# Optimization experiments

Hardware: AMD Instinct MI355X
Metric: run time of the kernel (lower is better)

The kernel has to match this reference:

```python
import jax, jax.numpy as jnp
import numpy as np

B, N, F_IN, F_OUT, OUT = 32, 1024, 128, 128, 1


def setup_inputs() -> dict:
    key = jax.random.key(0)
    k = jax.random.split(key, 6)
    A = jax.random.uniform(k[0], (B, N, N), dtype=jnp.float32)
    H = jax.random.normal(k[1], (B, N, F_IN), dtype=jnp.float32)
    W = jax.random.normal(k[2], (F_IN, F_OUT), dtype=jnp.float32)
    b = jax.random.normal(k[3], (F_OUT,), dtype=jnp.float32)
    fc_w = jax.random.normal(k[4], (OUT, F_OUT), dtype=jnp.float32)
    fc_b = jax.random.normal(k[5], (OUT,), dtype=jnp.float32)
    return {"A": A, "H": H, "W": W, "b": b, "fc_w": fc_w, "fc_b": fc_b}


def reference(A, H, W, b, fc_w, fc_b):
    n = A.shape[1]
    A_tilde = A + jnp.eye(n, dtype=A.dtype)          # [B,N,N] add self-loops
    d = jnp.sum(A_tilde, axis=1)                      # [B,N] degrees (col sums, matches torch dim=1)
    inv_sqrt_d = 1.0 / jnp.sqrt(d)                    # elementwise, equivalent to sqrt(inv(diag(d)))
    # D^-1/2 A_tilde D^-1/2 as row/col scaling (avoids diag_embed + matrix inverse)
    A_norm = inv_sqrt_d[:, :, None] * A_tilde * inv_sqrt_d[:, None, :]
    h = jax.nn.relu(jnp.einsum('bij,bjf,fo->bio', A_norm, H, W) + b)  # GCN layer
    pooled = jnp.sum(h, axis=1)                       # [B,F_OUT] sum pooling over nodes
    return pooled @ fc_w.T + fc_b                     # [B,OUT]
```

## Files before the change

kernel.cpp:

```cpp
#include <hip/hip_runtime.h>
#include <hip/hip_bf16.h>

#define NB 32
#define NN 1024
#define FF 128

typedef __attribute__((ext_vector_type(8))) short short8;
typedef __attribute__((ext_vector_type(4))) float f32x4;

static __device__ __forceinline__ unsigned short f2bf(float x) {
  unsigned int u = __float_as_uint(x);
  u += 0x7fffu + ((u >> 16) & 1u);
  return (unsigned short)(u >> 16);
}

static __device__ __forceinline__ unsigned long long pack4bf(float a, float b, float c, float d) {
  return (unsigned long long)f2bf(a)
       | ((unsigned long long)f2bf(b) << 16)
       | ((unsigned long long)f2bf(c) << 32)
       | ((unsigned long long)f2bf(d) << 48);
}

static __device__ __forceinline__ void gl16(const void* g, void* l) {
  __builtin_amdgcn_global_load_lds((const __attribute__((address_space(1))) void*)g,
                                   (__attribute__((address_space(3))) void*)l, 16, 0, 0);
}

__global__ __launch_bounds__(256) void k1_colsum_cvt(const float* __restrict__ A,
                                                     unsigned short* __restrict__ Ab,
                                                     float* __restrict__ partial) {
  int t = threadIdx.x;
  int s = blockIdx.x;
  int b = blockIdx.y;
  const float* base = A + (size_t)b * NN * NN + (size_t)(s * 64) * NN + (t << 2);
  unsigned short* obase = Ab + (size_t)b * NN * NN + (size_t)(s * 64) * NN + (t << 2);
  int jj = t << 2;
  bool diag_band = ((t >> 4) == s);
  float4 sum = make_float4(0.f, 0.f, 0.f, 0.f);
  #pragma unroll 8
  for (int i = 0; i < 64; ++i) {
    float4 v = *reinterpret_cast<const float4*>(base + (size_t)i * NN);
    if (diag_band) {
      int gi = (s << 6) + i;
      v.x += (gi == jj)     ? 1.f : 0.f;
      v.y += (gi == jj + 1) ? 1.f : 0.f;
      v.z += (gi == jj + 2) ? 1.f : 0.f;
      v.w += (gi == jj + 3) ? 1.f : 0.f;
    }
    sum.x += v.x; sum.y += v.y; sum.z += v.z; sum.w += v.w;
    *reinterpret_cast<unsigned long long*>(obase + (size_t)i * NN) =
        pack4bf(v.x, v.y, v.z, v.w);
  }
  *reinterpret_cast<float4*>(partial + (((b << 4) + s) << 10) + jj) = sum;
}

__global__ __launch_bounds__(512) void k3_hw(const float* __restrict__ H,
                                             const float* __restrict__ W,
                                             const float* __restrict__ partial,
                                             unsigned short* __restrict__ HWpT) {
  __shared__ unsigned short Ws[128][136];
  __shared__ unsigned short Hs[128][136];
  __shared__ float isdJ[128];
  int jblk = blockIdx.x;
  int b = blockIdx.y;
  int tid = threadIdx.x, wave = tid >> 6, lane = tid & 63;

  if (tid < 128) {
    float d = 0.f;
    #pragma unroll
    for (int s = 0; s < 16; ++s) d += partial[(((b << 4) + s) << 10) + (jblk << 7) + tid];
    isdJ[tid] = rsqrtf(d);
  }
  #pragma unroll
  for (int p = 0; p < 8; ++p) {
    int idx = (p << 11) + (tid << 2);
    int k = idx >> 7, o = idx & 127;
    const float4 w = *reinterpret_cast<const float4*>(W + idx);
    Ws[o    ][k] = f2bf(w.x);
    Ws[o + 1][k] = f2bf(w.y);
    Ws[o + 2][k] = f2bf(w.z);
    Ws[o + 3][k] = f2bf(w.w);
  }
  {
    int r = tid >> 5, c = (tid & 31) << 2;
    const float* Hbase = H + (size_t)b * NN * FF + (size_t)(jblk * 128) * FF;
    #pragma unroll
    for (int p = 0; p < 8; ++p) {
      int row = r + (p << 4);
      const float4 v = *reinterpret_cast<const float4*>(Hbase + (size_t)row * FF + c);
      *reinterpret_cast<unsigned long long*>(&Hs[row][c]) = pack4bf(v.x, v.y, v.z, v.w);
    }
  }
  __syncthreads();

  f32x4 acc[8];
  #pragma unroll
  for (int i = 0; i < 8; ++i) acc[i] = (f32x4){0.f, 0.f, 0.f, 0.f};

  int mrow = (wave << 4) + (lane & 15);
  int koff = (lane >> 4) << 3;
  #pragma unroll
  for (int kk = 0; kk < 4; ++kk) {
    short8 af = *reinterpret_cast<const short8*>(&Ws[mrow][(kk << 5) + koff]);
    #pragma unroll
    for (int nf = 0; nf < 8; ++nf) {
      short8 bf = *reinterpret_cast<const short8*>(&Hs[(nf << 4) + (lane & 15)][(kk << 5) + koff]);
      acc[nf] = __builtin_amdgcn_mfma_f32_16x16x32_bf16(af, bf, acc[nf], 0, 0, 0);
    }
  }

  int q = lane >> 4, l15 = lane & 15;
  __syncthreads();
  #pragma unroll
  for (int nf = 0; nf < 8; ++nf) {
    int jl = (nf << 4) + l15;
    float sc = isdJ[jl];
    #pragma unroll
    for (int r = 0; r < 4; ++r) {
      Ws[(wave << 4) + (q << 2) + r][jl] = f2bf(acc[nf][r] * sc);
    }
  }
  __syncthreads();
  {
    unsigned short* obase = HWpT + (size_t)b * FF * NN + (size_t)(jblk * 128);
    int c8 = (tid & 15) << 3;
    #pragma unroll
    for (int p = 0; p < 4; ++p) {
      int o = (p << 5) + (tid >> 4);
      *reinterpret_cast<short8*>(obase + (size_t)o * NN + c8) =
          *reinterpret_cast<const short8*>(&Ws[o][c8]);
    }
  }
}

__global__ __launch_bounds__(256) void k4_gcn(const unsigned short* __restrict__ Ab,
                                              const unsigned short* __restrict__ HWpT,
                                              const float* __restrict__ partial,
                                              const float* __restrict__ bias,
                                              float* __restrict__ pooled_part) {
  __shared__ __align__(1024) char ldsA[3 * 8192];
  __shared__ __align__(16) float ldsIsd[64];
  __shared__ float ldsRed[2][128];
  int fid = blockIdx.x;
  int nid = (fid & 7) * 64 + (fid >> 3);
  int b = nid >> 4, iblk = nid & 15;
  int i0 = iblk << 6;
  int tid = threadIdx.x, wave = tid >> 6, lane = tid & 63;
  int wm = wave >> 1, wn = wave & 1;
  int l15 = lane & 15, q = lane >> 4;
  int q16 = q << 4;

  if (tid < 64) {
    float d = 0.f;
    #pragma unroll
    for (int s = 0; s < 16; ++s) d += partial[(((b << 4) + s) << 10) + i0 + tid];
    ldsIsd[tid] = rsqrtf(d);
  }

  int r8 = lane >> 3;
  int ch = (lane & 7) ^ r8;
  const unsigned short* aS = Ab + (size_t)b * NN * NN
                           + (size_t)(i0 + (wave << 4) + r8) * NN + (ch << 3);
  const unsigned short* bS = HWpT + (size_t)b * FF * NN
                           + (size_t)((wn << 6) + l15) * NN + (q << 3);

  f32x4 acc[2][4];
  #pragma unroll
  for (int m = 0; m < 2; ++m)
    #pragma unroll
    for (int n = 0; n < 4; ++n) acc[m][n] = (f32x4){0.f, 0.f, 0.f, 0.f};

  int swzR = (l15 & 7) << 4;
  int offA[2];
  #pragma unroll
  for (int mr = 0; mr < 2; ++mr)
    offA[mr] = ((wm << 5) + (mr << 4) + l15) * 128 + q16;

  short8 breg[2][4][2];

#define STAGE_A(buf, k0) { \
    const unsigned short* s_ = aS + (k0); \
    char* d_ = ldsA + (buf) * 8192 + (wave << 11); \
    gl16(s_,          d_); \
    gl16(s_ + 8 * NN, d_ + 1024); }

#define LOAD_B(slot, k0) { \
    _Pragma("unroll") \
    for (int nf_ = 0; nf_ < 4; ++nf_) { \
      _Pragma("unroll") \
      for (int kk_ = 0; kk_ < 2; ++kk_) \
        breg[slot][nf_][kk_] = *reinterpret_cast<const short8*>( \
            bS + (size_t)(nf_ << 4) * NN + (k0) + (kk_ << 5)); } }

  STAGE_A(0, 0)
  LOAD_B(0, 0)
  STAGE_A(1, 64)

  #pragma unroll
  for (int t = 0; t < 16; ++t) {
    if (t < 15) LOAD_B((t + 1) & 1, (t + 1) * 64)
    if (t < 14) STAGE_A((t + 2) % 3, (t + 2) * 64)
    if (t < 14)       asm volatile("s_waitcnt vmcnt(12)" ::: "memory");
    else if (t == 14) asm volatile("s_waitcnt vmcnt(10)" ::: "memory");
    else              asm volatile("s_waitcnt vmcnt(0)" ::: "memory");
    __builtin_amdgcn_s_barrier();
    const char* Abuf = ldsA + (t % 3) * 8192;
    #pragma unroll
    for (int kk = 0; kk < 2; ++kk) {
      short8 af[2];
      #pragma unroll
      for (int mr = 0; mr < 2; ++mr)
        af[mr] = *reinterpret_cast<const short8*>(Abuf + ((offA[mr] + (kk << 6)) ^ swzR));
      #pragma unroll
      for (int mr = 0; mr < 2; ++mr)
        #pragma unroll
        for (int nf = 0; nf < 4; ++nf)
          acc[mr][nf] = __builtin_amdgcn_mfma_f32_16x16x32_bf16(
              af[mr], breg[t & 1][nf][kk], acc[mr][nf], 0, 0, 0);
    }
    __builtin_amdgcn_s_barrier();
  }
#undef STAGE_A
#undef LOAD_B

  #pragma unroll
  for (int nf = 0; nf < 4; ++nf) {
    int f = (wn << 6) + (nf << 4) + l15;
    float bi = bias[f];
    float stot = 0.f;
    #pragma unroll
    for (int mr = 0; mr < 2; ++mr) {
      const f32x4 sc = *reinterpret_cast<const f32x4*>(&ldsIsd[(wm << 5) + (mr << 4) + (q << 2)]);
      stot += fmaxf(acc[mr][nf][0] * sc[0] + bi, 0.f)
            + fmaxf(acc[mr][nf][1] * sc[1] + bi, 0.f)
            + fmaxf(acc[mr][nf][2] * sc[2] + bi, 0.f)
            + fmaxf(acc[mr][nf][3] * sc[3] + bi, 0.f);
    }
    stot += __shfl_xor(stot, 16);
    stot += __shfl_xor(stot, 32);
    if (lane < 16) ldsRed[wm][f] = stot;
  }
  __syncthreads();
  if (tid < 128)
    pooled_part[(((b << 4) + iblk) << 7) + tid] = ldsRed[0][tid] + ldsRed[1][tid];
}

__global__ void k5_out(const float* __restrict__ pp, const float* __restrict__ fcw,
                       const float* __restrict__ fcb, float* __restrict__ out) {
  int b = blockIdx.x, t = threadIdx.x;
  float s = 0.f;
  #pragma unroll
  for (int slot = 0; slot < 16; ++slot) {
    const float* p = pp + (((b << 4) + slot) << 7);
    s += p[t] * fcw[t] + p[t + 64] * fcw[t + 64];
  }
  #pragma unroll
  for (int off = 1; off < 64; off <<= 1) s += __shfl_xor(s, off);
  if (t == 0) out[b] = s + fcb[0];
}

extern "C" void kernel_launch(void* const* d_in, const int* in_sizes, int n_in,
                              void* d_out, int out_size, void* d_ws, size_t ws_size,
                              hipStream_t stream) {
  const float* A    = (const float*)d_in[0];
  const float* H    = (const float*)d_in[1];
  const float* W    = (const float*)d_in[2];
  const float* bias = (const float*)d_in[3];
  const float* fcw  = (const float*)d_in[4];
  const float* fcb  = (const float*)d_in[5];
  float* out = (float*)d_out;

  float* ws = (float*)d_ws;
  float* partial     = ws;
  float* pooled_part = ws + 524288;
  unsigned short* HWpT = (unsigned short*)(ws + 524288 + 65536);
  unsigned short* Ab   = HWpT + (size_t)NB * FF * NN;

  k1_colsum_cvt<<<dim3(16, 32), 256, 0, stream>>>(A, Ab, partial);
  k3_hw        <<<dim3(8, 32), 512, 0, stream>>>(H, W, partial, HWpT);
  k4_gcn       <<<512, 256, 0, stream>>>(Ab, HWpT, partial, bias, pooled_part);
  k5_out       <<<32, 64, 0, stream>>>(pooled_part, fcw, fcb, out);
}
```

Baseline: 80.54 us.

## Replace triple-buffered A/register-B pipeline with single-buffer LDS staging for both operands

The main GCN GEMM kernel drops its manual triple-buffered LDS pipeline for A and its double-buffered register prefetch of B. Both A and the transposed HW tiles are now staged into single LDS buffers via global_load_lds, with a __syncthreads before and after each k-step. The wave tiling changes from 2x2 (32x64 per wave) to 4x1 (16 rows by all 128 features per wave), and launch bounds request 2 blocks per CU to raise occupancy. This relies on occupancy rather than explicit prefetch to hide latency, at the cost of serialized load and compute within each block and more LDS reads for B.

```diff
diff --git a/kernel.cpp b/kernel.cpp
--- a/kernel.cpp
+++ b/kernel.cpp
@@ -133,22 +133,21 @@
   }
 }
 
-__global__ __launch_bounds__(256) void k4_gcn(const unsigned short* __restrict__ Ab,
-                                              const unsigned short* __restrict__ HWpT,
-                                              const float* __restrict__ partial,
-                                              const float* __restrict__ bias,
-                                              float* __restrict__ pooled_part) {
-  __shared__ __align__(1024) char ldsA[3 * 8192];
+__global__ __launch_bounds__(256, 2) void k4_gcn(const unsigned short* __restrict__ Ab,
+                                                 const unsigned short* __restrict__ HWpT,
+                                                 const float* __restrict__ partial,
+                                                 const float* __restrict__ bias,
+                                                 float* __restrict__ pooled_part) {
+  __shared__ __align__(1024) unsigned short As[64 * 64];
+  __shared__ __align__(1024) unsigned short Bs[128 * 64];
   __shared__ __align__(16) float ldsIsd[64];
-  __shared__ float ldsRed[2][128];
+  __shared__ float ldsRed[4][128];
   int fid = blockIdx.x;
   int nid = (fid & 7) * 64 + (fid >> 3);
   int b = nid >> 4, iblk = nid & 15;
   int i0 = iblk << 6;
   int tid = threadIdx.x, wave = tid >> 6, lane = tid & 63;
-  int wm = wave >> 1, wn = wave & 1;
   int l15 = lane & 15, q = lane >> 4;
-  int q16 = q << 4;
 
   if (tid < 64) {
     float d = 0.f;
@@ -157,92 +156,61 @@
     ldsIsd[tid] = rsqrtf(d);
   }
 
+  f32x4 acc[8];
+  #pragma unroll
+  for (int i = 0; i < 8; ++i) acc[i] = (f32x4){0.f, 0.f, 0.f, 0.f};
+
   int r8 = lane >> 3;
-  int ch = (lane & 7) ^ r8;
+  int schunk = (lane & 7) ^ r8;
   const unsigned short* aS = Ab + (size_t)b * NN * NN
-                           + (size_t)(i0 + (wave << 4) + r8) * NN + (ch << 3);
+                           + (size_t)(i0 + (wave << 4) + r8) * NN + (schunk << 3);
   const unsigned short* bS = HWpT + (size_t)b * FF * NN
-                           + (size_t)((wn << 6) + l15) * NN + (q << 3);
-
-  f32x4 acc[2][4];
-  #pragma unroll
-  for (int m = 0; m < 2; ++m)
-    #pragma unroll
-    for (int n = 0; n < 4; ++n) acc[m][n] = (f32x4){0.f, 0.f, 0.f, 0.f};
-
-  int swzR = (l15 & 7) << 4;
-  int offA[2];
-  #pragma unroll
-  for (int mr = 0; mr < 2; ++mr)
-    offA[mr] = ((wm << 5) + (mr << 4) + l15) * 128 + q16;
-
-  short8 breg[2][4][2];
-
-#define STAGE_A(buf, k0) { \
-    const unsigned short* s_ = aS + (k0); \
-    char* d_ = ldsA + (buf) * 8192 + (wave << 11); \
-    gl16(s_,          d_); \
-    gl16(s_ + 8 * NN, d_ + 1024); }
-
-#define LOAD_B(slot, k0) { \
-    _Pragma("unroll") \
-    for (int nf_ = 0; nf_ < 4; ++nf_) { \
-      _Pragma("unroll") \
-      for (int kk_ = 0; kk_ < 2; ++kk_) \
-        breg[slot][nf_][kk_] = *reinterpret_cast<const short8*>( \
-            bS + (size_t)(nf_ << 4) * NN + (k0) + (kk_ << 5)); } }
-
-  STAGE_A(0, 0)
-  LOAD_B(0, 0)
-  STAGE_A(1, 64)
-
-  #pragma unroll
-  for (int t = 0; t < 16; ++t) {
-    if (t < 15) LOAD_B((t + 1) & 1, (t + 1) * 64)
-    if (t < 14) STAGE_A((t + 2) % 3, (t + 2) * 64)
-    if (t < 14)       asm volatile("s_waitcnt vmcnt(12)" ::: "memory");
-    else if (t == 14) asm volatile("s_waitcnt vmcnt(10)" ::: "memory");
-    else              asm volatile("s_waitcnt vmcnt(0)" ::: "memory");
-    __builtin_amdgcn_s_barrier();
-    const char* Abuf = ldsA + (t % 3) * 8192;
+                           + (size_t)((wave << 5) + r8) * NN + (schunk << 3);
+  char* asBase = (char*)As + (wave << 11);
+  char* bsBase = (char*)Bs + (wave << 12);
+  int mrow = (wave << 4) + l15;
+  int q16 = q << 4;
+  int aoff0 = (mrow * 128 + q16) ^ ((mrow & 7) << 4);
+
+  for (int k0 = 0; k0 < NN; k0 += 64) {
+    gl16(aS + k0,           asBase);
+    gl16(aS + k0 + 8 * NN,  asBase + 1024);
+    gl16(bS + k0,           bsBase);
+    gl16(bS + k0 + 8 * NN,  bsBase + 1024);
+    gl16(bS + k0 + 16 * NN, bsBase + 2048);
+    gl16(bS + k0 + 24 * NN, bsBase + 3072);
+    __syncthreads();
     #pragma unroll
     for (int kk = 0; kk < 2; ++kk) {
-      short8 af[2];
+      const short8 af = *reinterpret_cast<const short8*>((const char*)As + (aoff0 ^ (kk << 6)));
       #pragma unroll
-      for (int mr = 0; mr < 2; ++mr)
-        af[mr] = *reinterpret_cast<const short8*>(Abuf + ((offA[mr] + (kk << 6)) ^ swzR));
-      #pragma unroll
-      for (int mr = 0; mr < 2; ++mr)
-        #pragma unroll
-        for (int nf = 0; nf < 4; ++nf)
-          acc[mr][nf] = __builtin_amdgcn_mfma_f32_16x16x32_bf16(
-              af[mr], breg[t & 1][nf][kk], acc[mr][nf], 0, 0, 0);
-    }
-    __builtin_amdgcn_s_barrier();
-  }
-#undef STAGE_A
-#undef LOAD_B
-
-  #pragma unroll
-  for (int nf = 0; nf < 4; ++nf) {
-    int f = (wn << 6) + (nf << 4) + l15;
+      for (int nf = 0; nf < 8; ++nf) {
+        int br = (nf << 4) + l15;
+        const short8 bf = *reinterpret_cast<const short8*>(
+            (const char*)Bs + ((br * 128 + (kk << 6) + q16) ^ ((br & 7) << 4)));
+        acc[nf] = __builtin_amdgcn_mfma_f32_16x16x32_bf16(af, bf, acc[nf], 0, 0, 0);
+      }
+    }
+    __syncthreads();
+  }
+
+  const f32x4 sc = *reinterpret_cast<const f32x4*>(&ldsIsd[(wave << 4) + (q << 2)]);
+  #pragma unroll
+  for (int nf = 0; nf < 8; ++nf) {
+    int f = (nf << 4) + l15;
     float bi = bias[f];
-    float stot = 0.f;
-    #pragma unroll
-    for (int mr = 0; mr < 2; ++mr) {
-      const f32x4 sc = *reinterpret_cast<const f32x4*>(&ldsIsd[(wm << 5) + (mr << 4) + (q << 2)]);
-      stot += fmaxf(acc[mr][nf][0] * sc[0] + bi, 0.f)
-            + fmaxf(acc[mr][nf][1] * sc[1] + bi, 0.f)
-            + fmaxf(acc[mr][nf][2] * sc[2] + bi, 0.f)
-            + fmaxf(acc[mr][nf][3] * sc[3] + bi, 0.f);
-    }
-    stot += __shfl_xor(stot, 16);
-    stot += __shfl_xor(stot, 32);
-    if (lane < 16) ldsRed[wm][f] = stot;
+    float s = fmaxf(acc[nf][0] * sc[0] + bi, 0.f)
+            + fmaxf(acc[nf][1] * sc[1] + bi, 0.f)
+            + fmaxf(acc[nf][2] * sc[2] + bi, 0.f)
+            + fmaxf(acc[nf][3] * sc[3] + bi, 0.f);
+    s += __shfl_xor(s, 16);
+    s += __shfl_xor(s, 32);
+    if (lane < 16) ldsRed[wave][f] = s;
   }
   __syncthreads();
   if (tid < 128)
-    pooled_part[(((b << 4) + iblk) << 7) + tid] = ldsRed[0][tid] + ldsRed[1][tid];
+    pooled_part[(((b << 4) + iblk) << 7) + tid] =
+        ldsRed[0][tid] + ldsRed[1][tid] + ldsRed[2][tid] + ldsRed[3][tid];
 }
 
 __global__ void k5_out(const float* __restrict__ pp, const float* __restrict__ fcw,
```

New measurement: 66.15 us. -17.9%, faster.

## Stage both A and HW tiles through LDS with double buffering in GCN kernel

Applied to the files above, without the earlier changes.

The main GCN matmul kernel previously streamed A tiles into LDS with a 3-deep buffer and loaded the transposed HW operand straight into registers. Now both operands go through LDS via global_load_lds with 2-deep buffering, and a full vmcnt(0) wait plus barrier closes each k-step. This is meant to cut per-thread global loads and VGPR pressure, with launch bounds set to 2 blocks per SM. In exchange, pipeline depth is lower and the full drain every iteration may expose memory latency.

```diff
diff --git a/kernel.cpp b/kernel.cpp
--- a/kernel.cpp
+++ b/kernel.cpp
@@ -133,14 +133,15 @@
   }
 }
 
-__global__ __launch_bounds__(256) void k4_gcn(const unsigned short* __restrict__ Ab,
-                                              const unsigned short* __restrict__ HWpT,
-                                              const float* __restrict__ partial,
-                                              const float* __restrict__ bias,
-                                              float* __restrict__ pooled_part) {
-  __shared__ __align__(1024) char ldsA[3 * 8192];
+__global__ __launch_bounds__(256, 2) void k4_gcn(const unsigned short* __restrict__ Ab,
+                                                 const unsigned short* __restrict__ HWpT,
+                                                 const float* __restrict__ partial,
+                                                 const float* __restrict__ bias,
+                                                 float* __restrict__ pooled_part) {
+  __shared__ __align__(1024) unsigned short As[2][64 * 64];
+  __shared__ __align__(1024) unsigned short Bs[2][128 * 64];
   __shared__ __align__(16) float ldsIsd[64];
-  __shared__ float ldsRed[2][128];
+  __shared__ float ldsRed[4][64];
   int fid = blockIdx.x;
   int nid = (fid & 7) * 64 + (fid >> 3);
   int b = nid >> 4, iblk = nid & 15;
@@ -157,80 +158,75 @@
     ldsIsd[tid] = rsqrtf(d);
   }
 
+  f32x4 acc[2][4];
+  #pragma unroll
+  for (int m = 0; m < 2; ++m)
+    #pragma unroll
+    for (int n = 0; n < 4; ++n) acc[m][n] = (f32x4){0.f, 0.f, 0.f, 0.f};
+
   int r8 = lane >> 3;
-  int ch = (lane & 7) ^ r8;
+  int schunk = (lane & 7) ^ r8;
   const unsigned short* aS = Ab + (size_t)b * NN * NN
-                           + (size_t)(i0 + (wave << 4) + r8) * NN + (ch << 3);
+                           + (size_t)(i0 + (wave << 4) + r8) * NN + (schunk << 3);
   const unsigned short* bS = HWpT + (size_t)b * FF * NN
-                           + (size_t)((wn << 6) + l15) * NN + (q << 3);
-
-  f32x4 acc[2][4];
-  #pragma unroll
-  for (int m = 0; m < 2; ++m)
-    #pragma unroll
-    for (int n = 0; n < 4; ++n) acc[m][n] = (f32x4){0.f, 0.f, 0.f, 0.f};
+                           + (size_t)((wave << 5) + r8) * NN + (schunk << 3);
 
   int swzR = (l15 & 7) << 4;
-  int offA[2];
-  #pragma unroll
-  for (int mr = 0; mr < 2; ++mr)
-    offA[mr] = ((wm << 5) + (mr << 4) + l15) * 128 + q16;
-
-  short8 breg[2][4][2];
-
-#define STAGE_A(buf, k0) { \
-    const unsigned short* s_ = aS + (k0); \
-    char* d_ = ldsA + (buf) * 8192 + (wave << 11); \
-    gl16(s_,          d_); \
-    gl16(s_ + 8 * NN, d_ + 1024); }
-
-#define LOAD_B(slot, k0) { \
-    _Pragma("unroll") \
-    for (int nf_ = 0; nf_ < 4; ++nf_) { \
-      _Pragma("unroll") \
-      for (int kk_ = 0; kk_ < 2; ++kk_) \
-        breg[slot][nf_][kk_] = *reinterpret_cast<const short8*>( \
-            bS + (size_t)(nf_ << 4) * NN + (k0) + (kk_ << 5)); } }
-
-  STAGE_A(0, 0)
-  LOAD_B(0, 0)
-  STAGE_A(1, 64)
+  int offA0 = (((wm << 5) + l15) << 7) + q16;
+  int offB0 = (((wn << 6) + l15) << 7) + q16;
+
+#define STAGE(buf, k0) { \
+    const unsigned short* sa_ = aS + (k0); \
+    const unsigned short* sb_ = bS + (k0); \
+    char* da_ = (char*)As + (buf) * 8192 + (wave << 11); \
+    char* db_ = (char*)Bs + (buf) * 16384 + (wave << 12); \
+    gl16(sa_,           da_); \
+    gl16(sa_ + 8 * NN,  da_ + 1024); \
+    gl16(sb_,           db_); \
+    gl16(sb_ + 8 * NN,  db_ + 1024); \
+    gl16(sb_ + 16 * NN, db_ + 2048); \
+    gl16(sb_ + 24 * NN, db_ + 3072); }
+
+  STAGE(0, 0)
+  asm volatile("s_waitcnt vmcnt(0)" ::: "memory");
+  __builtin_amdgcn_s_barrier();
 
   #pragma unroll
   for (int t = 0; t < 16; ++t) {
-    if (t < 15) LOAD_B((t + 1) & 1, (t + 1) * 64)
-    if (t < 14) STAGE_A((t + 2) % 3, (t + 2) * 64)
-    if (t < 14)       asm volatile("s_waitcnt vmcnt(12)" ::: "memory");
-    else if (t == 14) asm volatile("s_waitcnt vmcnt(10)" ::: "memory");
-    else              asm volatile("s_waitcnt vmcnt(0)" ::: "memory");
-    __builtin_amdgcn_s_barrier();
-    const char* Abuf = ldsA + (t % 3) * 8192;
+    if (t < 15) STAGE((t + 1) & 1, (t + 1) * 64)
+    const char* Abuf = (const char*)As + (t & 1) * 8192;
+    const char* Bbuf = (const char*)Bs + (t & 1) * 16384;
     #pragma unroll
     for (int kk = 0; kk < 2; ++kk) {
-      short8 af[2];
+      short8 af[2], bf[4];
       #pragma unroll
       for (int mr = 0; mr < 2; ++mr)
-        af[mr] = *reinterpret_cast<const short8*>(Abuf + ((offA[mr] + (kk << 6)) ^ swzR));
+        af[mr] = *reinterpret_cast<const short8*>(
+            Abuf + ((offA0 + (mr << 11) + (kk << 6)) ^ swzR));
+      #pragma unroll
+      for (int nf = 0; nf < 4; ++nf)
+        bf[nf] = *reinterpret_cast<const short8*>(
+            Bbuf + ((offB0 + (nf << 11) + (kk << 6)) ^ swzR));
       #pragma unroll
       for (int mr = 0; mr < 2; ++mr)
         #pragma unroll
         for (int nf = 0; nf < 4; ++nf)
-          acc[mr][nf] = __builtin_amdgcn_mfma_f32_16x16x32_bf16(
-              af[mr], breg[t & 1][nf][kk], acc[mr][nf], 0, 0, 0);
-    }
+          acc[mr][nf] = __builtin_amdgcn_mfma_f32_16x16x32_bf16(af[mr], bf[nf], acc[mr][nf], 0, 0, 0);
+    }
+    asm volatile("s_waitcnt vmcnt(0)" ::: "memory");
     __builtin_amdgcn_s_barrier();
   }
-#undef STAGE_A
-#undef LOAD_B
+#undef STAGE
 
   #pragma unroll
   for (int nf = 0; nf < 4; ++nf) {
-    int f = (wn << 6) + (nf << 4) + l15;
-    float bi = bias[f];
+    int fl = (nf << 4) + l15;
+    float bi = bias[(wn << 6) + fl];
     float stot = 0.f;
     #pragma unroll
     for (int mr = 0; mr < 2; ++mr) {
-      const f32x4 sc = *reinterpret_cast<const f32x4*>(&ldsIsd[(wm << 5) + (mr << 4) + (q << 2)]);
+      const f32x4 sc = *reinterpret_cast<const f32x4*>(
+          &ldsIsd[(wm << 5) + (mr << 4) + (q << 2)]);
       stot += fmaxf(acc[mr][nf][0] * sc[0] + bi, 0.f)
             + fmaxf(acc[mr][nf][1] * sc[1] + bi, 0.f)
             + fmaxf(acc[mr][nf][2] * sc[2] + bi, 0.f)
@@ -238,11 +234,14 @@
     }
     stot += __shfl_xor(stot, 16);
     stot += __shfl_xor(stot, 32);
-    if (lane < 16) ldsRed[wm][f] = stot;
-  }
-  __syncthreads();
-  if (tid < 128)
-    pooled_part[(((b << 4) + iblk) << 7) + tid] = ldsRed[0][tid] + ldsRed[1][tid];
+    if (lane < 16) ldsRed[wave][fl] = stot;
+  }
+  __syncthreads();
+  if (tid < 128) {
+    int wnf = tid >> 6, fl = tid & 63;
+    pooled_part[(((b << 4) + iblk) << 7) + tid] =
+        ldsRed[wnf][fl] + ldsRed[wnf + 2][fl];
+  }
 }
 
 __global__ void k5_out(const float* __restrict__ pp, const float* __restrict__ fcw,
```

Measured after the change: 66.68 us. -17.2%, faster.
